# Kernel optimization log

Hardware: AMD Instinct MI355X
Metric: run time of the kernel (lower is better)

## Reference

```python
import jax, jax.numpy as jnp
import numpy as np

NUM_CLASSES = 5
B, D, H, W = 4, 64, 256, 256


def _per_class_counts(labels, weights, num_classes):
    # labels: [B, N] int, weights: [B, N] float -> [B, C] float counts
    b = labels.shape[0]
    ids = labels + jnp.arange(b, dtype=labels.dtype)[:, None] * num_classes
    counts = jax.ops.segment_sum(weights.ravel(), ids.ravel().astype(jnp.int32),
                                 num_segments=b * num_classes)
    return counts.reshape(b, num_classes)


def _dice(predicted, target, num_classes):
    b = predicted.shape[0]
    p = predicted.reshape(b, -1)  # [B, N] integer class labels
    t = target.reshape(b, -1)
    ones = jnp.ones(p.shape, dtype=jnp.float32)
    pred_sum = _per_class_counts(p, ones, num_classes)                      # sum of one-hot(pred) over voxels
    tar_sum = _per_class_counts(t, ones, num_classes)                       # sum of one-hot(target) over voxels
    inter = _per_class_counts(p, (p == t).astype(jnp.float32), num_classes) # per-class intersection counts
    num = 2.0 * inter
    den = pred_sum + tar_sum
    zero = den == 0
    num = jnp.where(zero, 1.0, num)
    den = jnp.where(zero, 1.0, den)
    return (num / den).mean(axis=0)  # [C]


def setup_inputs() -> dict:
    key = jax.random.key(0)
    k1, k2 = jax.random.split(key)
    predicted = jax.random.randint(k1, (B, D, H, W), 0, NUM_CLASSES, dtype=jnp.int32)
    target = jax.random.randint(k2, (B, D, H, W), 0, NUM_CLASSES, dtype=jnp.int32)
    return {"predicted": predicted, "target": target}


def reference(predicted, target):
    return _dice(predicted, target, NUM_CLASSES)
```

## Files before the change

### kernel.cpp

```cpp
#include <hip/hip_runtime.h>

#define NUM_CLASSES 5
#define BATCH 4
#define NPB (64 * 256 * 256)
#define VEC_PER_BATCH (NPB / 4)
#define THREADS 256
#define VECS_PER_THREAD 8
#define BLOCKS_X (VEC_PER_BATCH / (THREADS * VECS_PER_THREAD))
#define SLOTS 15


__global__ __launch_bounds__(THREADS, 8) void dice_count_kernel(
    const int* __restrict__ pred, const int* __restrict__ targ,
    unsigned int* __restrict__ cnt) {
  const int b = blockIdx.y;
  const int4* __restrict__ p4 = (const int4*)(pred + (long long)b * NPB);
  const int4* __restrict__ t4 = (const int4*)(targ + (long long)b * NPB);

  const int base = blockIdx.x * (THREADS * VECS_PER_THREAD);

  unsigned int accP = 0, accT = 0, accI = 0;

#define ACC_ELEM(PE, TE)                                 \
  {                                                      \
    const unsigned sp = 6u * (unsigned)(PE);             \
    const unsigned st = 6u * (unsigned)(TE);             \
    const unsigned op = 1u << sp;                        \
    accP += op;                                          \
    accT += 1u << st;                                    \
    accI += ((PE) == (TE)) ? op : 0u;                    \
  }

#pragma unroll
  for (int k = 0; k < VECS_PER_THREAD; ++k) {
    const int idx = base + k * THREADS + threadIdx.x;
    const int4 pv = p4[idx];
    const int4 tv = t4[idx];
    ACC_ELEM(pv.x, tv.x)
    ACC_ELEM(pv.y, tv.y)
    ACC_ELEM(pv.z, tv.z)
    ACC_ELEM(pv.w, tv.w)
  }

  unsigned p01 = (accP & 63u) | (((accP >> 6) & 63u) << 16);
  unsigned p23 = ((accP >> 12) & 63u) | (((accP >> 18) & 63u) << 16);
  unsigned p4r = (accP >> 24) & 63u;
  unsigned t01 = (accT & 63u) | (((accT >> 6) & 63u) << 16);
  unsigned t23 = ((accT >> 12) & 63u) | (((accT >> 18) & 63u) << 16);
  unsigned t4r = (accT >> 24) & 63u;
  unsigned i01 = (accI & 63u) | (((accI >> 6) & 63u) << 16);
  unsigned i23 = ((accI >> 12) & 63u) | (((accI >> 18) & 63u) << 16);
  unsigned i4r = (accI >> 24) & 63u;

#pragma unroll
  for (int off = 32; off >= 1; off >>= 1) {
    p01 += (unsigned)__shfl_xor((int)p01, off);
    p23 += (unsigned)__shfl_xor((int)p23, off);
    p4r += (unsigned)__shfl_xor((int)p4r, off);
    t01 += (unsigned)__shfl_xor((int)t01, off);
    t23 += (unsigned)__shfl_xor((int)t23, off);
    t4r += (unsigned)__shfl_xor((int)t4r, off);
    i01 += (unsigned)__shfl_xor((int)i01, off);
    i23 += (unsigned)__shfl_xor((int)i23, off);
    i4r += (unsigned)__shfl_xor((int)i4r, off);
  }

  __shared__ unsigned int s[SLOTS];
  if (threadIdx.x < SLOTS) s[threadIdx.x] = 0;
  __syncthreads();

  if ((threadIdx.x & 63) == 0) {
    atomicAdd(&s[0], p01 & 0xFFFFu);
    atomicAdd(&s[1], p01 >> 16);
    atomicAdd(&s[2], p23 & 0xFFFFu);
    atomicAdd(&s[3], p23 >> 16);
    atomicAdd(&s[4], p4r);
    atomicAdd(&s[5], t01 & 0xFFFFu);
    atomicAdd(&s[6], t01 >> 16);
    atomicAdd(&s[7], t23 & 0xFFFFu);
    atomicAdd(&s[8], t23 >> 16);
    atomicAdd(&s[9], t4r);
    atomicAdd(&s[10], i01 & 0xFFFFu);
    atomicAdd(&s[11], i01 >> 16);
    atomicAdd(&s[12], i23 & 0xFFFFu);
    atomicAdd(&s[13], i23 >> 16);
    atomicAdd(&s[14], i4r);
  }
  __syncthreads();

  if (threadIdx.x < SLOTS)
    atomicAdd(&cnt[b * SLOTS + threadIdx.x], s[threadIdx.x]);
}

__global__ void dice_final_kernel(const unsigned int* __restrict__ cnt,
                                  float* __restrict__ out) {
  const int c = threadIdx.x;
  if (c < NUM_CLASSES) {
    float acc = 0.0f;
#pragma unroll
    for (int b = 0; b < BATCH; ++b) {
      const float ps = (float)cnt[b * SLOTS + c];
      const float ts = (float)cnt[b * SLOTS + 5 + c];
      const float is = (float)cnt[b * SLOTS + 10 + c];
      float num = 2.0f * is;
      float den = ps + ts;
      if (den == 0.0f) { num = 1.0f; den = 1.0f; }
      acc += num / den;
    }
    out[c] = acc * (1.0f / BATCH);
  }
}

extern "C" void kernel_launch(void* const* d_in, const int* in_sizes, int n_in,
                              void* d_out, int out_size, void* d_ws, size_t ws_size,
                              hipStream_t stream) {
  const int* pred = (const int*)d_in[0];
  const int* targ = (const int*)d_in[1];
  float* out = (float*)d_out;
  unsigned int* cnt = (unsigned int*)d_ws;

  hipMemsetAsync(cnt, 0, BATCH * SLOTS * sizeof(unsigned int), stream);

  dim3 grid(BLOCKS_X, BATCH);
  dice_count_kernel<<<grid, THREADS, 0, stream>>>(pred, targ, cnt);
  dice_final_kernel<<<1, 64, 0, stream>>>(cnt, out);
}
```

Before: 149.4 us.

## Double per-thread work, batch loads, replace global atomics with per-block partials

```diff
diff --git a/kernel.cpp b/kernel.cpp
--- a/kernel.cpp
+++ b/kernel.cpp
@@ -5,52 +5,61 @@
 #define NPB (64 * 256 * 256)
 #define VEC_PER_BATCH (NPB / 4)
 #define THREADS 256
-#define VECS_PER_THREAD 8
-#define BLOCKS_X (VEC_PER_BATCH / (THREADS * VECS_PER_THREAD))
+#define VECS 16
+#define CHUNK 8
+#define BLOCKS_X (VEC_PER_BATCH / (THREADS * VECS))
+#define TOTAL_BLOCKS (BLOCKS_X * BATCH)
 #define SLOTS 15
+#define PSTRIDE 16
 
 
-__global__ __launch_bounds__(THREADS, 8) void dice_count_kernel(
+__global__ __launch_bounds__(THREADS, 4) void dice_count_kernel(
     const int* __restrict__ pred, const int* __restrict__ targ,
-    unsigned int* __restrict__ cnt) {
+    unsigned int* __restrict__ partial) {
   const int b = blockIdx.y;
   const int4* __restrict__ p4 = (const int4*)(pred + (long long)b * NPB);
   const int4* __restrict__ t4 = (const int4*)(targ + (long long)b * NPB);
 
-  const int base = blockIdx.x * (THREADS * VECS_PER_THREAD);
+  const int base = blockIdx.x * (THREADS * VECS) + threadIdx.x;
 
-  unsigned int accP = 0, accT = 0, accI = 0;
+  unsigned accP[2] = {0, 0}, accT[2] = {0, 0}, accI[2] = {0, 0};
 
-#define ACC_ELEM(PE, TE)                                 \
-  {                                                      \
-    const unsigned sp = 6u * (unsigned)(PE);             \
-    const unsigned st = 6u * (unsigned)(TE);             \
-    const unsigned op = 1u << sp;                        \
-    accP += op;                                          \
-    accT += 1u << st;                                    \
-    accI += ((PE) == (TE)) ? op : 0u;                    \
+#pragma unroll
+  for (int h = 0; h < 2; ++h) {
+    int4 pv[CHUNK], tv[CHUNK];
+#pragma unroll
+    for (int k = 0; k < CHUNK; ++k) {
+      const int idx = base + (h * CHUNK + k) * THREADS;
+      pv[k] = p4[idx];
+      tv[k] = t4[idx];
+    }
+    unsigned aP = 0, aT = 0, aI = 0;
+#define ACC_ELEM(PE, TE)                               \
+    {                                                  \
+      const unsigned op = 1u << (6u * (unsigned)(PE)); \
+      aP += op;                                        \
+      aT += 1u << (6u * (unsigned)(TE));               \
+      aI += ((PE) == (TE)) ? op : 0u;                  \
+    }
+#pragma unroll
+    for (int k = 0; k < CHUNK; ++k) {
+      ACC_ELEM(pv[k].x, tv[k].x)
+      ACC_ELEM(pv[k].y, tv[k].y)
+      ACC_ELEM(pv[k].z, tv[k].z)
+      ACC_ELEM(pv[k].w, tv[k].w)
+    }
+    accP[h] = aP; accT[h] = aT; accI[h] = aI;
   }
 
-#pragma unroll
-  for (int k = 0; k < VECS_PER_THREAD; ++k) {
-    const int idx = base + k * THREADS + threadIdx.x;
-    const int4 pv = p4[idx];
-    const int4 tv = t4[idx];
-    ACC_ELEM(pv.x, tv.x)
-    ACC_ELEM(pv.y, tv.y)
-    ACC_ELEM(pv.z, tv.z)
-    ACC_ELEM(pv.w, tv.w)
-  }
-
-  unsigned p01 = (accP & 63u) | (((accP >> 6) & 63u) << 16);
-  unsigned p23 = ((accP >> 12) & 63u) | (((accP >> 18) & 63u) << 16);
-  unsigned p4r = (accP >> 24) & 63u;
-  unsigned t01 = (accT & 63u) | (((accT >> 6) & 63u) << 16);
-  unsigned t23 = ((accT >> 12) & 63u) | (((accT >> 18) & 63u) << 16);
-  unsigned t4r = (accT >> 24) & 63u;
-  unsigned i01 = (accI & 63u) | (((accI >> 6) & 63u) << 16);
-  unsigned i23 = ((accI >> 12) & 63u) | (((accI >> 18) & 63u) << 16);
-  unsigned i4r = (accI >> 24) & 63u;
+#define UNPACK(A, R01, R23, R4)                                          \
+  unsigned R01 = ((A[0] & 63u) + (A[1] & 63u)) |                         \
+                 ((((A[0] >> 6) & 63u) + ((A[1] >> 6) & 63u)) << 16);    \
+  unsigned R23 = (((A[0] >> 12) & 63u) + ((A[1] >> 12) & 63u)) |         \
+                 ((((A[0] >> 18) & 63u) + ((A[1] >> 18) & 63u)) << 16);  \
+  unsigned R4 = ((A[0] >> 24) & 63u) + ((A[1] >> 24) & 63u);
+  UNPACK(accP, p01, p23, p4r)
+  UNPACK(accT, t01, t23, t4r)
+  UNPACK(accI, i01, i23, i4r)
 
 #pragma unroll
   for (int off = 32; off >= 1; off >>= 1) {
@@ -89,25 +98,35 @@
   __syncthreads();
 
   if (threadIdx.x < SLOTS)
-    atomicAdd(&cnt[b * SLOTS + threadIdx.x], s[threadIdx.x]);
+    partial[(b * BLOCKS_X + blockIdx.x) * PSTRIDE + threadIdx.x] = s[threadIdx.x];
 }
 
-__global__ void dice_final_kernel(const unsigned int* __restrict__ cnt,
+__global__ void dice_final_kernel(const unsigned int* __restrict__ partial,
                                   float* __restrict__ out) {
-  const int c = threadIdx.x;
-  if (c < NUM_CLASSES) {
+  __shared__ unsigned int tot[BATCH * SLOTS];
+  const int t = threadIdx.x;
+  if (t < BATCH * SLOTS) {
+    const int slot = t % SLOTS;
+    const int bb = t / SLOTS;
+    unsigned int sum = 0;
+    for (int j = 0; j < BLOCKS_X; ++j)
+      sum += partial[(bb * BLOCKS_X + j) * PSTRIDE + slot];
+    tot[t] = sum;
+  }
+  __syncthreads();
+  if (t < NUM_CLASSES) {
     float acc = 0.0f;
 #pragma unroll
-    for (int b = 0; b < BATCH; ++b) {
-      const float ps = (float)cnt[b * SLOTS + c];
-      const float ts = (float)cnt[b * SLOTS + 5 + c];
-      const float is = (float)cnt[b * SLOTS + 10 + c];
+    for (int bb = 0; bb < BATCH; ++bb) {
+      const float ps = (float)tot[bb * SLOTS + t];
+      const float ts = (float)tot[bb * SLOTS + 5 + t];
+      const float is = (float)tot[bb * SLOTS + 10 + t];
       float num = 2.0f * is;
       float den = ps + ts;
       if (den == 0.0f) { num = 1.0f; den = 1.0f; }
       acc += num / den;
     }
-    out[c] = acc * (1.0f / BATCH);
+    out[t] = acc * (1.0f / BATCH);
   }
 }
 
@@ -117,11 +136,9 @@
   const int* pred = (const int*)d_in[0];
   const int* targ = (const int*)d_in[1];
   float* out = (float*)d_out;
-  unsigned int* cnt = (unsigned int*)d_ws;
-
-  hipMemsetAsync(cnt, 0, BATCH * SLOTS * sizeof(unsigned int), stream);
+  unsigned int* partial = (unsigned int*)d_ws;
 
   dim3 grid(BLOCKS_X, BATCH);
-  dice_count_kernel<<<grid, THREADS, 0, stream>>>(pred, targ, cnt);
-  dice_final_kernel<<<1, 64, 0, stream>>>(cnt, out);
+  dice_count_kernel<<<grid, THREADS, 0, stream>>>(pred, targ, partial);
+  dice_final_kernel<<<1, 64, 0, stream>>>(partial, out);
 }
```

Measured after the change: 152.9 us. 2.3% more time.
